# Optimization experiments

Measured on AMD Instinct MI355X. Metric: run time of the kernel, lower is better.

## Reference

```python
import jax, jax.numpy as jnp
import numpy as np

EMB = 1024
HEADS = 16
HEAD_SZ = EMB // HEADS
EPS = 1e-5


def _layernorm(x, g, b):
    mu = jnp.mean(x, axis=-1, keepdims=True)
    var = jnp.mean(jnp.square(x - mu), axis=-1, keepdims=True)
    return (x - mu) * jax.lax.rsqrt(var + EPS) * g + b


def setup_inputs() -> dict:
    key = jax.random.key(0)
    ks = jax.random.split(key, 12)
    s_in = 1.0 / np.sqrt(EMB)
    s_h = 1.0 / np.sqrt(4 * EMB)
    return {
        "x": jax.random.normal(ks[0], (4, 1024, EMB), jnp.float32),
        # per-head Q/K/V projections stacked: [H, EMB, HEAD_SZ], no bias
        "wq": jax.random.normal(ks[1], (HEADS, EMB, HEAD_SZ), jnp.float32) * s_in,
        "wk": jax.random.normal(ks[2], (HEADS, EMB, HEAD_SZ), jnp.float32) * s_in,
        "wv": jax.random.normal(ks[3], (HEADS, EMB, HEAD_SZ), jnp.float32) * s_in,
        "w_proj": jax.random.normal(ks[4], (EMB, EMB), jnp.float32) * s_in,
        "b_proj": jnp.zeros((EMB,), jnp.float32),
        "w1": jax.random.normal(ks[5], (EMB, 4 * EMB), jnp.float32) * s_in,
        "b1": jnp.zeros((4 * EMB,), jnp.float32),
        "w2": jax.random.normal(ks[6], (4 * EMB, EMB), jnp.float32) * s_h,
        "b2": jnp.zeros((EMB,), jnp.float32),
        "g1": jnp.ones((EMB,), jnp.float32),
        "be1": jnp.zeros((EMB,), jnp.float32),
        "g2": jnp.ones((EMB,), jnp.float32),
        "be2": jnp.zeros((EMB,), jnp.float32),
    }


def reference(x, wq, wk, wv, w_proj, b_proj, w1, b1, w2, b2, g1, be1, g2, be2):
    B, T, C = x.shape
    # --- self-attention (pre-norm) ---
    h = _layernorm(x, g1, be1)
    q = jnp.einsum("btc,hcd->bhtd", h, wq)
    k = jnp.einsum("btc,hcd->bhtd", h, wk)
    v = jnp.einsum("btc,hcd->bhtd", h, wv)
    scale = 1.0 / jnp.sqrt(jnp.asarray(HEAD_SZ, x.dtype))
    scores = jnp.einsum("bhtd,bhsd->bhts", q, k) * scale  # non-causal: SDPA called with no mask
    attn = jax.nn.softmax(scores, axis=-1)
    o = jnp.einsum("bhts,bhsd->bhtd", attn, v)
    o = o.transpose(0, 2, 1, 3).reshape(B, T, C)  # concat heads (same order as torch.cat)
    sa_out = o @ w_proj + b_proj
    x = x + sa_out
    # --- feed-forward; note ln2 applied twice, faithful to source ---
    t = _layernorm(x, g2, be2)
    t = _layernorm(t, g2, be2)
    ff = jax.nn.relu(t @ w1 + b1) @ w2 + b2
    return x + ff
```

## Files before the change

### kernel.cpp

```cpp
#include <hip/hip_runtime.h>
#include <hip/hip_bf16.h>
#include <math.h>
#include <stdint.h>

typedef __bf16 bf16_t;
typedef __bf16 bf16x4 __attribute__((ext_vector_type(4)));
typedef __bf16 bf16x8 __attribute__((ext_vector_type(8)));
typedef float floatx4 __attribute__((ext_vector_type(4)));

#define BM 128
#define BK 32

__device__ __forceinline__ size_t ftaddr(int m, int k, int KT) {
    return ((size_t)(m >> 4) * KT + (k >> 5)) * 512
         + (((k >> 3) & 3) * 16 + (m & 15)) * 8 + (k & 7);
}

__device__ __forceinline__ void gload16(const void* g, void* lds) {
    __builtin_amdgcn_global_load_lds(
        (__attribute__((address_space(1))) void*)(uintptr_t)g,
        (__attribute__((address_space(3))) void*)(uintptr_t)lds,
        16, 0, 0);
}

template<int N>
__device__ __forceinline__ void waitvm_barrier() {
    if constexpr (N == 0)       asm volatile("s_waitcnt vmcnt(0)\n\ts_barrier" ::: "memory");
    else if constexpr (N == 4)  asm volatile("s_waitcnt vmcnt(4)\n\ts_barrier" ::: "memory");
    else if constexpr (N == 6)  asm volatile("s_waitcnt vmcnt(6)\n\ts_barrier" ::: "memory");
    else if constexpr (N == 8)  asm volatile("s_waitcnt vmcnt(8)\n\ts_barrier" ::: "memory");
    else if constexpr (N == 12) asm volatile("s_waitcnt vmcnt(12)\n\ts_barrier" ::: "memory");
    else if constexpr (N == 16) asm volatile("s_waitcnt vmcnt(16)\n\ts_barrier" ::: "memory");
    else static_assert(N == 0, "unsupported vmcnt");
}

__device__ __forceinline__ void waitvm_barrier_rt(int n) {
    switch (n) {
    case 12: asm volatile("s_waitcnt vmcnt(12)\n\ts_barrier" ::: "memory"); break;
    case 8:  asm volatile("s_waitcnt vmcnt(8)\n\ts_barrier"  ::: "memory"); break;
    case 6:  asm volatile("s_waitcnt vmcnt(6)\n\ts_barrier"  ::: "memory"); break;
    case 4:  asm volatile("s_waitcnt vmcnt(4)\n\ts_barrier"  ::: "memory"); break;
    default: asm volatile("s_waitcnt vmcnt(0)\n\ts_barrier"  ::: "memory"); break;
    }
}

__global__ void prep_kernel(const float* __restrict__ wq, const float* __restrict__ wk,
                            const float* __restrict__ wv, const float* __restrict__ w_proj,
                            const float* __restrict__ w1, const float* __restrict__ w2,
                            bf16_t* __restrict__ WQKVT, bf16_t* __restrict__ WPROJT,
                            bf16_t* __restrict__ W1T, bf16_t* __restrict__ W2T,
                            const float* __restrict__ x, const float* __restrict__ g1,
                            const float* __restrict__ be1, bf16_t* __restrict__ HB)
{
    __shared__ __align__(16) char psm[33024];
    const int tid = threadIdx.x;
    if (blockIdx.x < 3072) {
        float (*tile)[65] = (float(*)[65])psm;
        const int idx = blockIdx.x;
        const float* in; bf16_t* out; int R, C, rt, ct; long nrow0;
        if (idx < 768) {
            const int z = idx >> 8;
            const int hd = (idx >> 4) & 15;
            rt = idx & 15; ct = 0; R = 1024; C = 64;
            in  = (z == 0 ? wq : z == 1 ? wk : wv) + hd * 65536;
            out = WQKVT; nrow0 = z * 1024 + hd * 64;
        } else if (idx < 1024) {
            const int t = idx - 768; rt = t & 15; ct = t >> 4; R = 1024; C = 1024;
            in = w_proj; out = WPROJT; nrow0 = 0;
        } else if (idx < 2048) {
            const int t = idx - 1024; rt = t & 15; ct = t >> 4; R = 1024; C = 4096;
            in = w1; out = W1T; nrow0 = 0;
        } else {
            const int t = idx - 2048; rt = t & 63; ct = t >> 6; R = 4096; C = 1024;
            in = w2; out = W2T; nrow0 = 0;
        }
        const int r0 = rt * 64, c0 = ct * 64;
        const int tr = tid >> 4;
        const int tc = (tid & 15) * 4;
#pragma unroll
        for (int rr = 0; rr < 4; rr++) {
            const int r = tr + rr * 16;
            const float4 v = *(const float4*)&in[(long)(r0 + r) * C + c0 + tc];
            tile[r][tc + 0] = v.x; tile[r][tc + 1] = v.y;
            tile[r][tc + 2] = v.z; tile[r][tc + 3] = v.w;
        }
        __syncthreads();
        const int KT = R >> 5;
        const int w = tid >> 6, l = tid & 63;
        const int c = l >> 4, rr2 = l & 15;
#pragma unroll
        for (int it = 0; it < 2; ++it) {
            const int t8 = it * 4 + w;
            const int kt = t8 >> 2;
            const int nb = t8 & 3;
            const long n = nrow0 + c0 + nb * 16 + rr2;
            const int k = r0 + kt * 32 + c * 8;
            bf16x8 o;
#pragma unroll
            for (int e = 0; e < 8; e++)
                o[e] = (bf16_t)tile[kt * 32 + c * 8 + e][nb * 16 + rr2];
            *(bf16x8*)&out[ftaddr((int)n, k, KT)] = o;
        }
    } else {
        bf16_t (*ybuf)[1032] = (bf16_t(*)[1032])psm;
        const int wave = tid >> 6, lane = tid & 63;
        const int rb = blockIdx.x - 3072;
        float4 gvv[4], bvv[4];
#pragma unroll
        for (int j = 0; j < 4; j++) {
            gvv[j] = ((const float4*)g1)[lane + j * 64];
            bvv[j] = ((const float4*)be1)[lane + j * 64];
        }
#pragma unroll
        for (int rr = 0; rr < 4; ++rr) {
            const int lrow = wave * 4 + rr;
            const float* xr = x + (size_t)(rb * 16 + lrow) * 1024;
            float4 v[4];
            float s = 0.f, s2 = 0.f;
#pragma unroll
            for (int j = 0; j < 4; j++) {
                v[j] = ((const float4*)xr)[lane + j * 64];
                s  += v[j].x + v[j].y + v[j].z + v[j].w;
                s2 += v[j].x * v[j].x + v[j].y * v[j].y + v[j].z * v[j].z + v[j].w * v[j].w;
            }
#pragma unroll
            for (int off = 32; off >= 1; off >>= 1) {
                s  += __shfl_xor(s, off);
                s2 += __shfl_xor(s2, off);
            }
            const float mu = s * (1.0f / 1024.0f);
            const float rs = rsqrtf(fmaxf(s2 * (1.0f / 1024.0f) - mu * mu, 0.f) + 1e-5f);
#pragma unroll
            for (int j = 0; j < 4; j++) {
                bf16x4 o;
                o[0] = (bf16_t)((v[j].x - mu) * rs * gvv[j].x + bvv[j].x);
                o[1] = (bf16_t)((v[j].y - mu) * rs * gvv[j].y + bvv[j].y);
                o[2] = (bf16_t)((v[j].z - mu) * rs * gvv[j].z + bvv[j].z);
                o[3] = (bf16_t)((v[j].w - mu) * rs * gvv[j].w + bvv[j].w);
                *(bf16x4*)&ybuf[lrow][(lane + j * 64) * 4] = o;
            }
        }
        __syncthreads();
        bf16_t* outBase = HB + (size_t)rb * 32 * 512;
#pragma unroll
        for (int it = 0; it < 8; ++it) {
            const int s = it * 256 + tid;
            const int kt = s >> 6, c = (s >> 4) & 3, rr2 = s & 15;
            const bf16x8 val = *(const bf16x8*)&ybuf[rr2][kt * 32 + c * 8];
            *(bf16x8*)&outBase[(size_t)s * 8] = val;
        }
    }
}

__global__ void ln2x_kernel(const float* __restrict__ x, const float* __restrict__ g,
                            const float* __restrict__ b, bf16_t* __restrict__ outb)
{
    __shared__ __align__(16) bf16_t ybuf[16][1032];
    const int tid = threadIdx.x, wave = tid >> 6, lane = tid & 63;
    const int rb = blockIdx.x;
    float4 gvv[4], bvv[4];
#pragma unroll
    for (int j = 0; j < 4; j++) {
        gvv[j] = ((const float4*)g)[lane + j * 64];
        bvv[j] = ((const float4*)b)[lane + j * 64];
    }
#pragma unroll
    for (int rr = 0; rr < 4; ++rr) {
        const int lrow = wave * 4 + rr;
        const float* xr = x + (size_t)(rb * 16 + lrow) * 1024;
        float4 v[4];
        float s = 0.f, s2 = 0.f;
#pragma unroll
        for (int j = 0; j < 4; j++) {
            v[j] = ((const float4*)xr)[lane + j * 64];
            s  += v[j].x + v[j].y + v[j].z + v[j].w;
            s2 += v[j].x * v[j].x + v[j].y * v[j].y + v[j].z * v[j].z + v[j].w * v[j].w;
        }
#pragma unroll
        for (int off = 32; off >= 1; off >>= 1) {
            s  += __shfl_xor(s, off);
            s2 += __shfl_xor(s2, off);
        }
        float mu = s * (1.0f / 1024.0f);
        float rs = rsqrtf(fmaxf(s2 * (1.0f / 1024.0f) - mu * mu, 0.f) + 1e-5f);
        s = 0.f; s2 = 0.f;
#pragma unroll
        for (int j = 0; j < 4; j++) {
            v[j].x = (v[j].x - mu) * rs * gvv[j].x + bvv[j].x;
            v[j].y = (v[j].y - mu) * rs * gvv[j].y + bvv[j].y;
            v[j].z = (v[j].z - mu) * rs * gvv[j].z + bvv[j].z;
            v[j].w = (v[j].w - mu) * rs * gvv[j].w + bvv[j].w;
            s  += v[j].x + v[j].y + v[j].z + v[j].w;
            s2 += v[j].x * v[j].x + v[j].y * v[j].y + v[j].z * v[j].z + v[j].w * v[j].w;
        }
#pragma unroll
        for (int off = 32; off >= 1; off >>= 1) {
            s  += __shfl_xor(s, off);
            s2 += __shfl_xor(s2, off);
        }
        mu = s * (1.0f / 1024.0f);
        rs = rsqrtf(fmaxf(s2 * (1.0f / 1024.0f) - mu * mu, 0.f) + 1e-5f);
#pragma unroll
        for (int j = 0; j < 4; j++) {
            bf16x4 o;
            o[0] = (bf16_t)((v[j].x - mu) * rs * gvv[j].x + bvv[j].x);
            o[1] = (bf16_t)((v[j].y - mu) * rs * gvv[j].y + bvv[j].y);
            o[2] = (bf16_t)((v[j].z - mu) * rs * gvv[j].z + bvv[j].z);
            o[3] = (bf16_t)((v[j].w - mu) * rs * gvv[j].w + bvv[j].w);
            *(bf16x4*)&ybuf[lrow][(lane + j * 64) * 4] = o;
        }
    }
    __syncthreads();
    bf16_t* outBase = outb + (size_t)rb * 32 * 512;
#pragma unroll
    for (int it = 0; it < 8; ++it) {
        const int s = it * 256 + tid;
        const int kt = s >> 6, c = (s >> 4) & 3, rr2 = s & 15;
        const bf16x8 val = *(const bf16x8*)&ybuf[rr2][kt * 32 + c * 8];
        *(bf16x8*)&outBase[(size_t)s * 8] = val;
    }
}

template<int EPI, int BNt, int DEPTH>
__global__ __launch_bounds__(256, 2)
void gemm_bt(const bf16_t* __restrict__ A, const bf16_t* __restrict__ Bt,
             const int K,
             const float* __restrict__ bias, const float* __restrict__ resid,
             float* __restrict__ outf, bf16_t* __restrict__ outb,
             bf16_t* __restrict__ aux1, bf16_t* __restrict__ aux2,
             const int Nout)
{
    constexpr int NFRAG = (BNt == 256) ? 8 : 4;
    constexpr int AI    = (BNt == 64) ? 2 : 4;
    constexpr int LPS   = (BNt == 256) ? 6 : (BNt == 128) ? 4 : 3;
    constexpr int BFT   = BNt / 16;
    constexpr int ASZ = DEPTH * 8 * 512;
    constexpr int BSZ = DEPTH * BFT * 512;
    __shared__ __align__(16) bf16_t smem[ASZ + BSZ];
    bf16_t* Asb = smem;
    bf16_t* Bsb = smem + ASZ;
    const int tid  = threadIdx.x;
    const int wave = tid >> 6, lane = tid & 63;
    const int wr = wave >> 1, wc = wave & 1;
    const int bm = blockIdx.x * BM, bn = blockIdx.y * BNt;
    const int KT = K >> 5;

    floatx4 acc[AI][NFRAG];
#pragma unroll
    for (int i = 0; i < AI; i++)
#pragma unroll
        for (int j = 0; j < NFRAG; j++) acc[i][j] = (floatx4){0.f, 0.f, 0.f, 0.f};

    const bf16_t* gA0 = A + ((size_t)(bm / 16 + wave * 2 + 0) * KT) * 512 + lane * 8;
    const bf16_t* gA1 = A + ((size_t)(bm / 16 + wave * 2 + 1) * KT) * 512 + lane * 8;
    const int lA0 = (wave * 2 + 0) * 512;
    const int lA1 = (wave * 2 + 1) * 512;

    const bf16_t* gB[4];
    int lB0 = 0;
    if (BNt == 256) {
#pragma unroll
        for (int q = 0; q < 4; q++)
            gB[q] = Bt + ((size_t)(bn / 16 + wave * 4 + q) * KT) * 512 + lane * 8;
    } else if (BNt == 128) {
        gB[0] = Bt + ((size_t)(bn / 16 + wave * 2 + 0) * KT) * 512 + lane * 8;
        gB[1] = Bt + ((size_t)(bn / 16 + wave * 2 + 1) * KT) * 512 + lane * 8;
    } else {
        gB[0] = Bt + ((size_t)(bn / 16 + wave) * KT) * 512 + lane * 8;
        lB0 = wave * 512;
    }

    auto stage = [&](int t, int bu) {
        const size_t off = (size_t)t * 512;
        gload16(gA0 + off, Asb + bu * 4096 + lA0);
        gload16(gA1 + off, Asb + bu * 4096 + lA1);
        if (BNt == 256) {
#pragma unroll
            for (int q = 0; q < 4; q++)
                gload16(gB[q] + off, Bsb + bu * (BFT * 512) + (wave * 4 + q) * 512);
        } else if (BNt == 128) {
            gload16(gB[0] + off, Bsb + bu * 4096 + lA0);
            gload16(gB[1] + off, Bsb + bu * 4096 + lA1);
        } else {
            gload16(gB[0] + off, Bsb + bu * (4 * 512) + lB0);
        }
    };

    auto compute = [&](int bu) {
        bf16x8 af[AI], bfv[NFRAG];
        if (BNt == 64) {
#pragma unroll
            for (int i = 0; i < AI; i++)
                af[i] = *(const bf16x8*)&Asb[bu * 4096 + (wave * 2 + i) * 512 + lane * 8];
#pragma unroll
            for (int j = 0; j < NFRAG; j++)
                bfv[j] = *(const bf16x8*)&Bsb[bu * (4 * 512) + j * 512 + lane * 8];
        } else {
#pragma unroll
            for (int i = 0; i < AI; i++)
                af[i] = *(const bf16x8*)&Asb[bu * 4096 + (wr * 4 + i) * 512 + lane * 8];
#pragma unroll
            for (int j = 0; j < NFRAG; j++)
                bfv[j] = *(const bf16x8*)&Bsb[bu * (BFT * 512) + (wc * NFRAG + j) * 512 + lane * 8];
        }
#pragma unroll
        for (int i = 0; i < AI; i++)
#pragma unroll
            for (int j = 0; j < NFRAG; j++)
                acc[i][j] = __builtin_amdgcn_mfma_f32_16x16x32_bf16(af[i], bfv[j], acc[i][j], 0, 0, 0);
    };

    const int NT = K / BK;
    if (BNt == 64) {
#pragma unroll
        for (int i = 0; i < DEPTH - 2; ++i) stage(i, i);
        int t = 0;
        for (; t + 5 < NT; t += 2) {
            waitvm_barrier<LPS * 2>();
            stage(t + 4, (t + 4) % DEPTH);
            compute(t % DEPTH);
            stage(t + 5, (t + 5) % DEPTH);
            compute((t + 1) % DEPTH);
        }
        waitvm_barrier<LPS * 2>();
        compute((NT - 4) % DEPTH);
        compute((NT - 3) % DEPTH);
        waitvm_barrier<0>();
        compute((NT - 2) % DEPTH);
        compute((NT - 1) % DEPTH);
    } else {
#pragma unroll
        for (int i = 0; i < DEPTH - 1; ++i) stage(i, i);
        int bu = 0;
        for (int t = 0; t <= NT - DEPTH; ++t) {
            waitvm_barrier<LPS * (DEPTH - 2)>();
            stage(t + DEPTH - 1, bu == 0 ? DEPTH - 1 : bu - 1);
            compute(bu);
            bu = (bu + 1 == DEPTH) ? 0 : bu + 1;
        }
#pragma unroll
        for (int j = DEPTH - 2; j >= 0; --j) {
            waitvm_barrier_rt(LPS * j);
            compute(bu);
            bu = (bu + 1 == DEPTH) ? 0 : bu + 1;
        }
    }

    const int er = (lane >> 4) * 4, ec = lane & 15;
    if constexpr (EPI == 0) {
        if (bn >= 2048) {
            __syncthreads();
            bf16_t* scr = smem;
#pragma unroll
            for (int i = 0; i < AI; i++)
#pragma unroll
                for (int j = 0; j < NFRAG; j++)
#pragma unroll
                    for (int r = 0; r < 4; r++)
                        scr[((wc * NFRAG + j) * 16 + ec) * 136 + (wr * 4 + i) * 16 + er + r] =
                            (bf16_t)acc[i][j][r];
            __syncthreads();
            const int bq = bm >> 10, tmod = bm & 1023, h0 = (bn - 2048) >> 6;
#pragma unroll
            for (int it = 0; it < 8; ++it) {
                const int c = it * 256 + tid;
                const int dl = c >> 4, t16 = c & 15;
                const bf16x8 val = *(const bf16x8*)&scr[dl * 136 + t16 * 8];
                const int h = h0 + (dl >> 6), dd = dl & 63;
                *(bf16x8*)&aux2[(size_t)((bq * 16 + h) * 64 + dd) * 1024 + tmod + t16 * 8] = val;
            }
            return;
        }
    }
#pragma unroll
    for (int i = 0; i < AI; i++) {
#pragma unroll
        for (int j = 0; j < NFRAG; j++) {
            const int col = (BNt == 64) ? (bn + j * 16 + ec)
                                        : (bn + (wc * NFRAG + j) * 16 + ec);
#pragma unroll
            for (int r = 0; r < 4; r++) {
                const int row = (BNt == 64) ? (bm + wave * 32 + i * 16 + er + r)
                                            : (bm + (wr * 4 + i) * 16 + er + r);
                const float v = acc[i][j][r];
                if (EPI == 0) {
                    const int b = row >> 10, t = row & 1023;
                    if (col < 1024) {
                        const int h = col >> 6, d = col & 63;
                        outb[(size_t)((b * 16 + h) * 1024 + t) * 64 + d] = (bf16_t)v;
                    } else {
                        const int c2 = col - 1024, h = c2 >> 6, d = c2 & 63;
                        aux1[(size_t)((b * 16 + h) * 1024 + t) * 64 + d] = (bf16_t)v;
                    }
                } else if (EPI == 1 || EPI == 3) {
                    const size_t idx = (size_t)row * Nout + col;
                    outf[idx] = v + bias[col] + resid[idx];
                } else if (EPI == 2) {
                    outb[ftaddr(row, col, Nout >> 5)] = (bf16_t)fmaxf(v + bias[col], 0.f);
                }
            }
        }
    }
}

__global__ __launch_bounds__(256, 4)
void attn_kernel(const bf16_t* __restrict__ Q, const bf16_t* __restrict__ Kg,
                 const bf16_t* __restrict__ Vt, bf16_t* __restrict__ Og)
{
    __shared__ __align__(16) bf16_t Ks[2][4096];
    __shared__ __align__(16) bf16_t Vs[2][4096];
    __shared__ __align__(16) bf16_t Ps[4][1024];
    const int tid = threadIdx.x, wave = tid >> 6, lane = tid & 63;
    const int lin = blockIdx.x + (blockIdx.y << 4);
    const int xcd = lin & 7, idx = lin >> 3;
    const int bh = xcd * 8 + (idx >> 4);
    const int qt = idx & 15;
    const int b = bh >> 4, h = bh & 15;
    const int q0 = qt * 64 + wave * 16;
    const bf16_t* Qb = Q + (size_t)bh * 65536;
    const char* Kb = (const char*)(Kg + (size_t)bh * 65536);
    const char* Vb = (const char*)(Vt + (size_t)bh * 65536);
    const int fr = lane & 15, g = lane >> 4, fk = g * 8;

    const bf16x8 qf0 = *(const bf16x8*)&Qb[(size_t)(q0 + fr) * 64 + fk];
    const bf16x8 qf1 = *(const bf16x8*)&Qb[(size_t)(q0 + fr) * 64 + 32 + fk];

    floatx4 o[4];
#pragma unroll
    for (int dt = 0; dt < 4; dt++) o[dt] = (floatx4){0.f, 0.f, 0.f, 0.f};
    float lsum[4] = {0.f, 0.f, 0.f, 0.f};
    bf16_t* pw = &Ps[wave][0];
    const float sscale = 0.125f * 1.44269504088896f;

    auto stage = [&](int s0, int bu) {
#pragma unroll
        for (int t = 0; t < 2; t++) {
            const int j = wave * 2 + t;
            gload16(Kb + (size_t)(s0 + lane) * 128 + j * 16, &Ks[bu][j * 512]);
            gload16(Vb + (size_t)lane * 2048 + (size_t)s0 * 2 + j * 16, &Vs[bu][j * 512]);
        }
    };

    stage(0, 0);
    int bu = 0;
    for (int it = 0; it < 16; ++it) {
        __syncthreads();
        if (it < 15) stage((it + 1) * 64, bu ^ 1);
        const bf16_t* Kl = Ks[bu];
        const bf16_t* Vl = Vs[bu];

        floatx4 sacc[4];
#pragma unroll
        for (int ss = 0; ss < 4; ss++) sacc[ss] = (floatx4){0.f, 0.f, 0.f, 0.f};
        __builtin_amdgcn_s_setprio(1);
#pragma unroll
        for (int ss = 0; ss < 4; ss++) {
#pragma unroll
            for (int c = 0; c < 2; c++) {
                const int ch = c * 4 + g;
                const bf16x8 qf = (c == 0) ? qf0 : qf1;
                const bf16x8 kf = *(const bf16x8*)&Kl[ch * 512 + (ss * 16 + fr) * 8];
                sacc[ss] = __builtin_amdgcn_mfma_f32_16x16x32_bf16(qf, kf, sacc[ss], 0, 0, 0);
            }
        }
        __builtin_amdgcn_s_setprio(0);
#pragma unroll
        for (int ss = 0; ss < 2; ss++) {
#pragma unroll
            for (int r = 0; r < 4; r++) {
                const float p = __builtin_amdgcn_exp2f(sacc[ss][r] * sscale);
                lsum[r] += p;
                const int q = g * 4 + r;
                pw[(ss * 2 + (fr >> 3)) * 128 + q * 8 + (fr & 7)] = (bf16_t)p;
            }
        }
        asm volatile("s_waitcnt lgkmcnt(0)" ::: "memory");
#pragma unroll
        for (int ss = 2; ss < 4; ss++) {
#pragma unroll
            for (int r = 0; r < 4; r++) {
                const float p = __builtin_amdgcn_exp2f(sacc[ss][r] * sscale);
                lsum[r] += p;
                const int q = g * 4 + r;
                pw[(ss * 2 + (fr >> 3)) * 128 + q * 8 + (fr & 7)] = (bf16_t)p;
            }
        }
        {
            const int ch = g;
            const bf16x8 pf = *(const bf16x8*)&pw[ch * 128 + fr * 8];
            __builtin_amdgcn_s_setprio(1);
#pragma unroll
            for (int dt = 0; dt < 4; dt++) {
                const bf16x8 vf = *(const bf16x8*)&Vl[ch * 512 + (dt * 16 + fr) * 8];
                o[dt] = __builtin_amdgcn_mfma_f32_16x16x32_bf16(pf, vf, o[dt], 0, 0, 0);
            }
            __builtin_amdgcn_s_setprio(0);
        }
        asm volatile("s_waitcnt lgkmcnt(0)" ::: "memory");
        {
            const int ch = 4 + g;
            const bf16x8 pf = *(const bf16x8*)&pw[ch * 128 + fr * 8];
            __builtin_amdgcn_s_setprio(1);
#pragma unroll
            for (int dt = 0; dt < 4; dt++) {
                const bf16x8 vf = *(const bf16x8*)&Vl[ch * 512 + (dt * 16 + fr) * 8];
                o[dt] = __builtin_amdgcn_mfma_f32_16x16x32_bf16(pf, vf, o[dt], 0, 0, 0);
            }
            __builtin_amdgcn_s_setprio(0);
        }
        asm volatile("" ::: "memory");
        bu ^= 1;
    }
#pragma unroll
    for (int r = 0; r < 4; r++) {
        float l = lsum[r];
        l += __shfl_xor(l, 1);
        l += __shfl_xor(l, 2);
        l += __shfl_xor(l, 4);
        l += __shfl_xor(l, 8);
        lsum[r] = 1.0f / l;
    }
    const int tq = q0 + g * 4;
#pragma unroll
    for (int dt = 0; dt < 4; dt++) {
#pragma unroll
        for (int r = 0; r < 4; r++) {
            const int m = b * 1024 + tq + r;
            const int k = h * 64 + dt * 16 + fr;
            Og[ftaddr(m, k, 32)] = (bf16_t)(o[dt][r] * lsum[r]);
        }
    }
}

extern "C" void kernel_launch(void* const* d_in, const int* in_sizes, int n_in,
                              void* d_out, int out_size, void* d_ws, size_t ws_size,
                              hipStream_t stream)
{
    const float* x      = (const float*)d_in[0];
    const float* wq     = (const float*)d_in[1];
    const float* wk     = (const float*)d_in[2];
    const float* wv     = (const float*)d_in[3];
    const float* w_proj = (const float*)d_in[4];
    const float* b_proj = (const float*)d_in[5];
    const float* w1     = (const float*)d_in[6];
    const float* b1     = (const float*)d_in[7];
    const float* w2     = (const float*)d_in[8];
    const float* b2     = (const float*)d_in[9];
    const float* g1     = (const float*)d_in[10];
    const float* be1    = (const float*)d_in[11];
    const float* g2     = (const float*)d_in[12];
    const float* be2    = (const float*)d_in[13];
    float* out = (float*)d_out;
    char* ws = (char*)d_ws;

    bf16_t* WQKVT = (bf16_t*)(ws + 0x0000000);
    bf16_t* WPROJT= (bf16_t*)(ws + 0x0600000);
    bf16_t* W1T   = (bf16_t*)(ws + 0x0800000);
    bf16_t* W2T   = (bf16_t*)(ws + 0x1000000);
    bf16_t* HB    = (bf16_t*)(ws + 0x1800000);
    bf16_t* Qb    = (bf16_t*)(ws + 0x2000000);
    bf16_t* Kb    = (bf16_t*)(ws + 0x2800000);
    bf16_t* Vtb   = (bf16_t*)(ws + 0x3000000);
    bf16_t* AO    = (bf16_t*)(ws + 0x3800000);
    float*  X2    = (float*)(ws + 0x4000000);
    bf16_t* TB    = (bf16_t*)(ws + 0x2800000);
    bf16_t* FF1B  = (bf16_t*)(ws + 0x5000000);

    dim3 blk(256);
    prep_kernel<<<3328, blk, 0, stream>>>(wq, wk, wv, w_proj, w1, w2,
                                          WQKVT, WPROJT, W1T, W2T,
                                          x, g1, be1, HB);
    gemm_bt<0, 128, 5><<<dim3(32, 24), blk, 0, stream>>>(HB, WQKVT, 1024, nullptr, nullptr,
                                                         nullptr, Qb, Kb, Vtb, 3072);
    attn_kernel<<<dim3(16, 64), blk, 0, stream>>>(Qb, Kb, Vtb, AO);
    gemm_bt<1, 64, 6><<<dim3(32, 16), blk, 0, stream>>>(AO, WPROJT, 1024, b_proj, x,
                                                        X2, nullptr, nullptr, nullptr, 1024);
    ln2x_kernel<<<256, blk, 0, stream>>>(X2, g2, be2, TB);
    gemm_bt<2, 256, 3><<<dim3(32, 16), blk, 0, stream>>>(TB, W1T, 1024, b1, nullptr,
                                                         nullptr, FF1B, nullptr, nullptr, 4096);
    gemm_bt<3, 64, 6><<<dim3(32, 16), blk, 0, stream>>>(FF1B, W2T, 4096, b2, X2,
                                                        out, nullptr, nullptr, nullptr, 1024);
}
```

Baseline: 291.4 us.

## Add register-staged A GEMM for narrow-N projection and FFN2 kernels

Adds a new gemm_ra kernel for the two 64-wide output GEMMs (attention projection and FFN down-projection). A tiles are loaded straight into registers four steps ahead with inline global_load_dwordx4, and only B tiles are staged through LDS in a 12-deep ring. The goal is to cut LDS traffic and capacity for A and to keep more loads in flight. The BNt==64 path is removed from gemm_bt. The manual vmcnt accounting and the wrapped prefetch indices (& NTm) are fragile and issue redundant loads at the tail.

New measurement: 297.7 us. 1.02x slower.

```diff
diff --git a/kernel.cpp b/kernel.cpp
--- a/kernel.cpp
+++ b/kernel.cpp
@@ -221,6 +221,96 @@
     }
 }
 
+template<int EPI>
+__global__ __launch_bounds__(256, 2)
+void gemm_ra(const bf16_t* __restrict__ A, const bf16_t* __restrict__ Bt,
+             const int K, const float* __restrict__ bias,
+             const float* __restrict__ resid, float* __restrict__ outf,
+             const int Nout)
+{
+    constexpr int D = 12;
+    __shared__ __align__(16) bf16_t Bs[D * 2048];
+    const int tid = threadIdx.x, wave = tid >> 6, lane = tid & 63;
+    const int bm = blockIdx.x * BM, bn = blockIdx.y * 64;
+    const int KT = K >> 5;
+    const int NT = K >> 5;
+    const int NTm = NT - 1;
+
+    floatx4 acc[2][4];
+#pragma unroll
+    for (int i = 0; i < 2; i++)
+#pragma unroll
+        for (int j = 0; j < 4; j++) acc[i][j] = (floatx4){0.f, 0.f, 0.f, 0.f};
+
+    const bf16_t* gA0 = A + ((size_t)(bm / 16 + wave * 2 + 0) * KT) * 512 + lane * 8;
+    const bf16_t* gA1 = A + ((size_t)(bm / 16 + wave * 2 + 1) * KT) * 512 + lane * 8;
+    const bf16_t* gB  = Bt + ((size_t)(bn / 16 + wave) * KT) * 512 + lane * 8;
+
+    auto stageB = [&](int t, int b) {
+        gload16(gB + (size_t)t * 512, Bs + b * 2048 + wave * 512);
+    };
+    auto loadA = [&](bf16x8& r0, bf16x8& r1, int t) {
+        const bf16_t* p0 = gA0 + (size_t)t * 512;
+        const bf16_t* p1 = gA1 + (size_t)t * 512;
+        asm volatile("global_load_dwordx4 %0, %1, off"
+                     : "=&v"(r0) : "v"(p0) : "memory");
+        asm volatile("global_load_dwordx4 %0, %1, off"
+                     : "=&v"(r1) : "v"(p1) : "memory");
+    };
+    auto computeS = [&](const bf16x8& a0, const bf16x8& a1, int b) {
+        bf16x8 bfv[4];
+#pragma unroll
+        for (int j = 0; j < 4; j++)
+            bfv[j] = *(const bf16x8*)&Bs[b * 2048 + j * 512 + lane * 8];
+#pragma unroll
+        for (int j = 0; j < 4; j++) {
+            acc[0][j] = __builtin_amdgcn_mfma_f32_16x16x32_bf16(a0, bfv[j], acc[0][j], 0, 0, 0);
+            acc[1][j] = __builtin_amdgcn_mfma_f32_16x16x32_bf16(a1, bfv[j], acc[1][j], 0, 0, 0);
+        }
+    };
+
+    bf16x8 R[4][2];
+#pragma unroll
+    for (int i = 0; i < 4; i++) loadA(R[i][0], R[i][1], i);
+#pragma unroll
+    for (int s = 0; s < 8; s++) stageB(s, s);
+    asm volatile("s_waitcnt vmcnt(4)\n\ts_barrier" ::: "memory");
+
+    int bu = 0;
+    const int NTI = NT >> 2;
+    for (int T = 0; T < NTI; T++) {
+        const int t = T << 2;
+        if (T) asm volatile("s_waitcnt vmcnt(12)\n\ts_barrier" ::: "memory");
+#pragma unroll
+        for (int i = 0; i < 4; i++) {
+            int bs = bu + 8 + i; if (bs >= D) bs -= D;
+            stageB((t + 8 + i) & NTm, bs);
+            asm volatile("s_waitcnt vmcnt(10)" ::: "memory");
+            __builtin_amdgcn_sched_barrier(0);
+            int bc = bu + i; if (bc >= D) bc -= D;
+            computeS(R[i][0], R[i][1], bc);
+            loadA(R[i][0], R[i][1], (t + 4 + i) & NTm);
+        }
+        bu += 4; if (bu >= D) bu -= D;
+    }
+    asm volatile("s_waitcnt vmcnt(0)" ::: "memory");
+
+    const int er = (lane >> 4) * 4, ec = lane & 15;
+#pragma unroll
+    for (int i = 0; i < 2; i++) {
+#pragma unroll
+        for (int j = 0; j < 4; j++) {
+            const int col = bn + j * 16 + ec;
+#pragma unroll
+            for (int r = 0; r < 4; r++) {
+                const int row = bm + wave * 32 + i * 16 + er + r;
+                const size_t idx = (size_t)row * Nout + col;
+                outf[idx] = acc[i][j][r] + bias[col] + resid[idx];
+            }
+        }
+    }
+}
+
 template<int EPI, int BNt, int DEPTH>
 __global__ __launch_bounds__(256, 2)
 void gemm_bt(const bf16_t* __restrict__ A, const bf16_t* __restrict__ Bt,
@@ -231,8 +321,8 @@
              const int Nout)
 {
     constexpr int NFRAG = (BNt == 256) ? 8 : 4;
-    constexpr int AI    = (BNt == 64) ? 2 : 4;
-    constexpr int LPS   = (BNt == 256) ? 6 : (BNt == 128) ? 4 : 3;
+    constexpr int AI    = 4;
+    constexpr int LPS   = (BNt == 256) ? 6 : 4;
     constexpr int BFT   = BNt / 16;
     constexpr int ASZ = DEPTH * 8 * 512;
     constexpr int BSZ = DEPTH * BFT * 512;
@@ -257,17 +347,13 @@
     const int lA1 = (wave * 2 + 1) * 512;
 
     const bf16_t* gB[4];
-    int lB0 = 0;
     if (BNt == 256) {
 #pragma unroll
         for (int q = 0; q < 4; q++)
             gB[q] = Bt + ((size_t)(bn / 16 + wave * 4 + q) * KT) * 512 + lane * 8;
-    } else if (BNt == 128) {
+    } else {
         gB[0] = Bt + ((size_t)(bn / 16 + wave * 2 + 0) * KT) * 512 + lane * 8;
         gB[1] = Bt + ((size_t)(bn / 16 + wave * 2 + 1) * KT) * 512 + lane * 8;
-    } else {
-        gB[0] = Bt + ((size_t)(bn / 16 + wave) * KT) * 512 + lane * 8;
-        lB0 = wave * 512;
     }
 
     auto stage = [&](int t, int bu) {
@@ -278,31 +364,20 @@
 #pragma unroll
             for (int q = 0; q < 4; q++)
                 gload16(gB[q] + off, Bsb + bu * (BFT * 512) + (wave * 4 + q) * 512);
-        } else if (BNt == 128) {
+        } else {
             gload16(gB[0] + off, Bsb + bu * 4096 + lA0);
             gload16(gB[1] + off, Bsb + bu * 4096 + lA1);
-        } else {
-            gload16(gB[0] + off, Bsb + bu * (4 * 512) + lB0);
         }
     };
 
     auto compute = [&](int bu) {
         bf16x8 af[AI], bfv[NFRAG];
-        if (BNt == 64) {
-#pragma unroll
-            for (int i = 0; i < AI; i++)
-                af[i] = *(const bf16x8*)&Asb[bu * 4096 + (wave * 2 + i) * 512 + lane * 8];
-#pragma unroll
-            for (int j = 0; j < NFRAG; j++)
-                bfv[j] = *(const bf16x8*)&Bsb[bu * (4 * 512) + j * 512 + lane * 8];
-        } else {
-#pragma unroll
-            for (int i = 0; i < AI; i++)
-                af[i] = *(const bf16x8*)&Asb[bu * 4096 + (wr * 4 + i) * 512 + lane * 8];
-#pragma unroll
-            for (int j = 0; j < NFRAG; j++)
-                bfv[j] = *(const bf16x8*)&Bsb[bu * (BFT * 512) + (wc * NFRAG + j) * 512 + lane * 8];
-        }
+#pragma unroll
+        for (int i = 0; i < AI; i++)
+            af[i] = *(const bf16x8*)&Asb[bu * 4096 + (wr * 4 + i) * 512 + lane * 8];
+#pragma unroll
+        for (int j = 0; j < NFRAG; j++)
+            bfv[j] = *(const bf16x8*)&Bsb[bu * (BFT * 512) + (wc * NFRAG + j) * 512 + lane * 8];
 #pragma unroll
         for (int i = 0; i < AI; i++)
 #pragma unroll
@@ -311,39 +386,20 @@
     };
 
     const int NT = K / BK;
-    if (BNt == 64) {
-#pragma unroll
-        for (int i = 0; i < DEPTH - 2; ++i) stage(i, i);
-        int t = 0;
-        for (; t + 5 < NT; t += 2) {
-            waitvm_barrier<LPS * 2>();
-            stage(t + 4, (t + 4) % DEPTH);
-            compute(t % DEPTH);
-            stage(t + 5, (t + 5) % DEPTH);
-            compute((t + 1) % DEPTH);
-        }
-        waitvm_barrier<LPS * 2>();
-        compute((NT - 4) % DEPTH);
-        compute((NT - 3) % DEPTH);
-        waitvm_barrier<0>();
-        compute((NT - 2) % DEPTH);
-        compute((NT - 1) % DEPTH);
-    } else {
-#pragma unroll
-        for (int i = 0; i < DEPTH - 1; ++i) stage(i, i);
-        int bu = 0;
-        for (int t = 0; t <= NT - DEPTH; ++t) {
-            waitvm_barrier<LPS * (DEPTH - 2)>();
-            stage(t + DEPTH - 1, bu == 0 ? DEPTH - 1 : bu - 1);
-            compute(bu);
-            bu = (bu + 1 == DEPTH) ? 0 : bu + 1;
-        }
-#pragma unroll
-        for (int j = DEPTH - 2; j >= 0; --j) {
-            waitvm_barrier_rt(LPS * j);
-            compute(bu);
-            bu = (bu + 1 == DEPTH) ? 0 : bu + 1;
-        }
+#pragma unroll
+    for (int i = 0; i < DEPTH - 1; ++i) stage(i, i);
+    int bu = 0;
+    for (int t = 0; t <= NT - DEPTH; ++t) {
+        waitvm_barrier<LPS * (DEPTH - 2)>();
+        stage(t + DEPTH - 1, bu == 0 ? DEPTH - 1 : bu - 1);
+        compute(bu);
+        bu = (bu + 1 == DEPTH) ? 0 : bu + 1;
+    }
+#pragma unroll
+    for (int j = DEPTH - 2; j >= 0; --j) {
+        waitvm_barrier_rt(LPS * j);
+        compute(bu);
+        bu = (bu + 1 == DEPTH) ? 0 : bu + 1;
     }
 
     const int er = (lane >> 4) * 4, ec = lane & 15;
@@ -376,12 +432,10 @@
     for (int i = 0; i < AI; i++) {
 #pragma unroll
         for (int j = 0; j < NFRAG; j++) {
-            const int col = (BNt == 64) ? (bn + j * 16 + ec)
-                                        : (bn + (wc * NFRAG + j) * 16 + ec);
+            const int col = bn + (wc * NFRAG + j) * 16 + ec;
 #pragma unroll
             for (int r = 0; r < 4; r++) {
-                const int row = (BNt == 64) ? (bm + wave * 32 + i * 16 + er + r)
-                                            : (bm + (wr * 4 + i) * 16 + er + r);
+                const int row = bm + (wr * 4 + i) * 16 + er + r;
                 const float v = acc[i][j][r];
                 if (EPI == 0) {
                     const int b = row >> 10, t = row & 1023;
@@ -392,9 +446,6 @@
                         const int c2 = col - 1024, h = c2 >> 6, d = c2 & 63;
                         aux1[(size_t)((b * 16 + h) * 1024 + t) * 64 + d] = (bf16_t)v;
                     }
-                } else if (EPI == 1 || EPI == 3) {
-                    const size_t idx = (size_t)row * Nout + col;
-                    outf[idx] = v + bias[col] + resid[idx];
                 } else if (EPI == 2) {
                     outb[ftaddr(row, col, Nout >> 5)] = (bf16_t)fmaxf(v + bias[col], 0.f);
                 }
@@ -573,11 +624,9 @@
     gemm_bt<0, 128, 5><<<dim3(32, 24), blk, 0, stream>>>(HB, WQKVT, 1024, nullptr, nullptr,
                                                          nullptr, Qb, Kb, Vtb, 3072);
     attn_kernel<<<dim3(16, 64), blk, 0, stream>>>(Qb, Kb, Vtb, AO);
-    gemm_bt<1, 64, 6><<<dim3(32, 16), blk, 0, stream>>>(AO, WPROJT, 1024, b_proj, x,
-                                                        X2, nullptr, nullptr, nullptr, 1024);
+    gemm_ra<1><<<dim3(32, 16), blk, 0, stream>>>(AO, WPROJT, 1024, b_proj, x, X2, 1024);
     ln2x_kernel<<<256, blk, 0, stream>>>(X2, g2, be2, TB);
     gemm_bt<2, 256, 3><<<dim3(32, 16), blk, 0, stream>>>(TB, W1T, 1024, b1, nullptr,
                                                          nullptr, FF1B, nullptr, nullptr, 4096);
-    gemm_bt<3, 64, 6><<<dim3(32, 16), blk, 0, stream>>>(FF1B, W2T, 4096, b2, X2,
-                                                        out, nullptr, nullptr, nullptr, 1024);
-}
+    gemm_ra<3><<<dim3(32, 16), blk, 0, stream>>>(FF1B, W2T, 4096, b2, X2, out, 1024);
+}
```
